# Performance work log

Measured on AMD Instinct MI355X. Metric: run time of the kernel, lower is better.

## Reference

```python
import jax, jax.numpy as jnp
import numpy as np

IN_FEATURES = 4096
OUT_FEATURES = 4096
NUM_CLUSTERS = 65536
CLUSTER_DIM = 4
DEFICIENCY = (CLUSTER_DIM - OUT_FEATURES % CLUSTER_DIM) % CLUSTER_DIM  # 0 here
INDEX_LEN = IN_FEATURES * (OUT_FEATURES + DEFICIENCY) // CLUSTER_DIM


def setup_inputs() -> dict:
    key = jax.random.key(0)
    k_x, k_c, k_i, k_b = jax.random.split(key, 4)
    x = jax.random.normal(k_x, (4, 2048, IN_FEATURES), dtype=jnp.float32)
    cluster = jax.random.normal(k_c, (NUM_CLUSTERS, CLUSTER_DIM), dtype=jnp.float32)
    index = jax.random.randint(k_i, (INDEX_LEN,), 0, NUM_CLUSTERS, dtype=jnp.int32)
    bias = jax.random.normal(k_b, (OUT_FEATURES,), dtype=jnp.float32)
    return {"x": x, "cluster": cluster, "index": index, "bias": bias}


def reference(x, cluster, index, bias):
    # Gather codebook vectors and reassemble the weight matrix [in, out(+pad)]
    vectors = cluster[index]                              # [INDEX_LEN, CLUSTER_DIM]
    weight = vectors.reshape(IN_FEATURES, -1)             # [in, out + deficiency]
    if DEFICIENCY > 0:
        weight = weight[:, :-DEFICIENCY]                  # crop padding columns
    # x: [B, S, in] @ weight: [in, out] -> [B, S, out]
    out = jnp.matmul(x, weight) + bias
    return out
```

## Files before the change

kernel.cpp:

```cpp
#include <hip/hip_runtime.h>
#include <hip/hip_bf16.h>
#include <stdint.h>

typedef unsigned short u16;
typedef __attribute__((ext_vector_type(8))) short bf16x8;
typedef __attribute__((ext_vector_type(4))) float f32x4;

#define KD 4096
#define ND 4096
#define MD 8192
#define NKT 64

__device__ __forceinline__ u16 f2bf(float f) {
    uint32_t u = __float_as_uint(f);
    u += 0x7FFFu + ((u >> 16) & 1u);
    return (u16)(u >> 16);
}

__device__ __forceinline__ void gload_lds16(const u16* g, u16* l) {
    __builtin_amdgcn_global_load_lds(
        (const __attribute__((address_space(1))) void*)g,
        (__attribute__((address_space(3))) void*)l, 16, 0, 0);
}

__global__ __launch_bounds__(256) void prep(
    const int* __restrict__ index, const float4* __restrict__ cluster4,
    u16* __restrict__ wt,
    const float4* __restrict__ x4, uint4* __restrict__ xb) {
    __shared__ int idx_s[64][32];
    const int bid = blockIdx.x;
    const int t   = threadIdx.x;
    if (bid < 2048) {
        const int k0 = (bid & 63) * 64;
        const int g0 = (bid >> 6) * 32;
        #pragma unroll
        for (int r = 0; r < 8; ++r) {
            int k = (t >> 5) + r * 8;
            int g = t & 31;
            idx_s[k][g] = index[(size_t)(k0 + k) * 1024 + g0 + g];
        }
        __syncthreads();
        const int g_local = t >> 3;
        const int k_local = (t & 7) * 8;
        u16 pk[4][8];
        #pragma unroll
        for (int j = 0; j < 8; ++j) {
            int idx = idx_s[k_local + j][g_local];
            float4 v = cluster4[idx];
            pk[0][j] = f2bf(v.x);
            pk[1][j] = f2bf(v.y);
            pk[2][j] = f2bf(v.z);
            pk[3][j] = f2bf(v.w);
        }
        const size_t nbase = (size_t)g0 * 4 + g_local * 4;
        #pragma unroll
        for (int c = 0; c < 4; ++c) {
            *reinterpret_cast<uint4*>(wt + (nbase + c) * KD + k0 + k_local) =
                *reinterpret_cast<const uint4*>(pk[c]);
        }
    } else {
        int i = (bid - 2048) * 256 + t;
        float4 a = x4[2 * i];
        float4 b = x4[2 * i + 1];
        u16 r[8] = {f2bf(a.x), f2bf(a.y), f2bf(a.z), f2bf(a.w),
                    f2bf(b.x), f2bf(b.y), f2bf(b.z), f2bf(b.w)};
        xb[i] = *reinterpret_cast<const uint4*>(r);
    }
}

__global__ __launch_bounds__(512, 2) void gemm256(
    const u16* __restrict__ A,
    const u16* __restrict__ Bt,
    const float* __restrict__ bias,
    float* __restrict__ C) {
    __shared__ __align__(16) u16 lds[65536];

    const int t    = threadIdx.x;
    const int lane = t & 63;
    const int wave = t >> 6;
    const int wm   = wave >> 2;
    const int wn   = wave & 3;

    const int bid = blockIdx.x;
    const int swz = (bid & 7) * 64 + (bid >> 3);
    const int n0  = (swz & 15) * 256;
    const int m0  = (swz >> 4) * 256;

    const u16* srcA[2]; const u16* srcB[2];
    #pragma unroll
    for (int i = 0; i < 2; ++i) {
        int p   = i * 8192 + t * 16;
        int row = p >> 7;
        int cb  = (p & 127) ^ ((row & 7) << 4);
        srcA[i] = A  + (size_t)(m0 + row) * KD + (cb >> 1);
        srcB[i] = Bt + (size_t)(n0 + row) * KD + (cb >> 1);
    }
    const size_t HS = (size_t)128 * KD;

    const int frow = lane & 15;
    int ce2[2];
    #pragma unroll
    for (int s = 0; s < 2; ++s)
        ce2[s] = ((s * 64 + ((lane >> 4) * 16)) ^ ((lane & 7) << 4)) >> 1;

    f32x4 acc[8][4] = {};
    bf16x8 aS[2][4][2];
    bf16x8 bR[2][2];

#define STAGE(isB, b, h, kt) do {                                          \
    _Pragma("unroll")                                                      \
    for (int i_ = 0; i_ < 2; ++i_) {                                       \
        const u16* s_ = ((isB) ? srcB[i_] : srcA[i_])                      \
                        + (size_t)(h) * HS + (kt) * 64;                    \
        u16* d_ = (u16*)lds + (b) * 32768 + (isB) * 16384                  \
                  + (h) * 8192 + i_ * 4096 + t * 8;                        \
        gload_lds16(s_, d_);                                               \
    } } while (0)

#define READA(b, mh) do {                                                  \
    _Pragma("unroll") for (int f_ = 0; f_ < 4; ++f_)                       \
    _Pragma("unroll") for (int s_ = 0; s_ < 2; ++s_)                       \
        aS[mh][f_][s_] = *(const bf16x8*)((u16*)lds + (b) * 32768 +        \
            ((wm * 128 + (mh) * 64 + f_ * 16 + frow) * 64) + ce2[s_]);     \
    } while (0)

#define READB(b, nh) do {                                                  \
    _Pragma("unroll") for (int g_ = 0; g_ < 2; ++g_)                       \
    _Pragma("unroll") for (int s_ = 0; s_ < 2; ++s_)                       \
        bR[g_][s_] = *(const bf16x8*)((u16*)lds + (b) * 32768 + 16384 +    \
            ((wn * 64 + (nh) * 32 + g_ * 16 + frow) * 64) + ce2[s_]);      \
    } while (0)

#define MFMA16(mh, nh) do {                                                \
    _Pragma("unroll") for (int f_ = 0; f_ < 4; ++f_)                       \
    _Pragma("unroll") for (int g_ = 0; g_ < 2; ++g_)                       \
    _Pragma("unroll") for (int s_ = 0; s_ < 2; ++s_)                       \
        acc[(mh)*4+f_][(nh)*2+g_] = __builtin_amdgcn_mfma_f32_16x16x32_bf16( \
            aS[mh][f_][s_], bR[g_][s_], acc[(mh)*4+f_][(nh)*2+g_], 0,0,0); \
    } while (0)

#define BAR() __builtin_amdgcn_s_barrier()
#define WAIT_LGKM() do { asm volatile("s_waitcnt lgkmcnt(0)" ::: "memory"); \
                         __builtin_amdgcn_sched_barrier(0); } while (0)
#define HINT_LGKM8() asm volatile("s_waitcnt lgkmcnt(8)" ::: "memory")
#define WAIT_VM4() asm volatile("s_waitcnt vmcnt(4)" ::: "memory")
#define PRIO1() __builtin_amdgcn_s_setprio(1)
#define PRIO0() __builtin_amdgcn_s_setprio(0)

    STAGE(0, 0, 0, 0);
    STAGE(0, 0, 1, 0);
    STAGE(1, 0, 0, 0);
    STAGE(1, 0, 1, 0);
    STAGE(1, 1, 0, 1);
    STAGE(0, 1, 0, 1);
    WAIT_VM4();
    BAR();

    for (int I = 0; I < NKT / 2; ++I) {
        const int tb  = 2 * I + 1;
        const int tp2 = (2 * I + 2) & (NKT - 1);
        const int tp3 = (2 * I + 3) & (NKT - 1);

        READA(0, 0); READB(0, 0); STAGE(0, 1, 1, tb);
        HINT_LGKM8();
        BAR(); WAIT_LGKM();
        PRIO1(); MFMA16(0, 0); PRIO0();
        READA(0, 1);
        BAR();
        STAGE(1, 1, 1, tb);
        BAR(); WAIT_LGKM();
        PRIO1(); MFMA16(1, 0); PRIO0();
        READB(0, 1);
        BAR();
        STAGE(1, 0, 0, tp2);
        BAR(); WAIT_LGKM();
        PRIO1(); MFMA16(0, 1); PRIO0();
        BAR();
        STAGE(0, 0, 0, tp2);
        BAR(); WAIT_LGKM();
        PRIO1(); MFMA16(1, 1); PRIO0();
        WAIT_VM4();
        BAR();
        READA(1, 0); READB(1, 0); STAGE(0, 0, 1, tp2);
        HINT_LGKM8();
        BAR(); WAIT_LGKM();
        PRIO1(); MFMA16(0, 0); PRIO0();
        READA(1, 1);
        BAR();
        STAGE(1, 0, 1, tp2);
        BAR(); WAIT_LGKM();
        PRIO1(); MFMA16(1, 0); PRIO0();
        READB(1, 1);
        BAR();
        STAGE(1, 1, 0, tp3);
        BAR(); WAIT_LGKM();
        PRIO1(); MFMA16(0, 1); PRIO0();
        BAR();
        STAGE(0, 1, 0, tp3);
        BAR(); WAIT_LGKM();
        PRIO1(); MFMA16(1, 1); PRIO0();
        WAIT_VM4();
        BAR();
    }

    const int crow = (lane >> 4) * 4;
    float bv[4];
    #pragma unroll
    for (int g = 0; g < 4; ++g)
        bv[g] = bias[n0 + wn * 64 + g * 16 + frow];
    #pragma unroll
    for (int f = 0; f < 8; ++f) {
        const int mrow = m0 + wm * 128 + f * 16 + crow;
        #pragma unroll
        for (int g = 0; g < 4; ++g) {
            float* cp = C + (size_t)mrow * ND + n0 + wn * 64 + g * 16 + frow;
            #pragma unroll
            for (int r = 0; r < 4; ++r)
                cp[(size_t)r * ND] = acc[f][g][r] + bv[g];
        }
    }
#undef STAGE
#undef READA
#undef READB
#undef MFMA16
#undef BAR
#undef WAIT_LGKM
#undef HINT_LGKM8
#undef WAIT_VM4
}

__global__ __launch_bounds__(256) void fallback_gemm(
    const float* __restrict__ x, const float4* __restrict__ cluster4,
    const int* __restrict__ index, const float* __restrict__ bias,
    float* __restrict__ out) {
    const int m = blockIdx.y;
    const int g = blockIdx.x * 256 + threadIdx.x;
    const float* xr = x + (size_t)m * KD;
    float a0 = 0.f, a1 = 0.f, a2 = 0.f, a3 = 0.f;
    for (int k = 0; k < KD; ++k) {
        float xv = xr[k];
        float4 cv = cluster4[index[(size_t)k * 1024 + g]];
        a0 += xv * cv.x; a1 += xv * cv.y; a2 += xv * cv.z; a3 += xv * cv.w;
    }
    size_t o = (size_t)m * ND + (size_t)g * 4;
    out[o + 0] = a0 + bias[g * 4 + 0];
    out[o + 1] = a1 + bias[g * 4 + 1];
    out[o + 2] = a2 + bias[g * 4 + 2];
    out[o + 3] = a3 + bias[g * 4 + 3];
}

extern "C" void kernel_launch(void* const* d_in, const int* in_sizes, int n_in,
                              void* d_out, int out_size, void* d_ws, size_t ws_size,
                              hipStream_t stream) {
    const float* x       = (const float*)d_in[0];
    const float* cluster = (const float*)d_in[1];
    const int*   index   = (const int*)d_in[2];
    const float* bias    = (const float*)d_in[3];
    float* out = (float*)d_out;

    const size_t WT_BYTES = (size_t)ND * KD * sizeof(u16);
    const size_t XB_BYTES = (size_t)MD * KD * sizeof(u16);

    if (ws_size >= WT_BYTES + XB_BYTES) {
        u16* wt = (u16*)d_ws;
        u16* xb = (u16*)((char*)d_ws + WT_BYTES);
        prep<<<2048 + (MD * KD / 8) / 256, 256, 0, stream>>>(
            index, (const float4*)cluster, wt, (const float4*)x, (uint4*)xb);
        gemm256<<<dim3((MD / 256) * (ND / 256)), 512, 0, stream>>>(
            xb, wt, bias, out);
    } else {
        fallback_gemm<<<dim3(1024 / 256, MD), 256, 0, stream>>>(
            x, (const float4*)cluster, index, bias, out);
    }
}
```

Before: 272.1 us.

## Fuse fp32-to-bf16 activation conversion into GEMM A-tile loading

Removes the separate pass that converted x to bf16 in workspace. The GEMM now loads fp32 x rows into registers, converts them to bf16 and writes swizzled tiles to LDS, interleaved with the existing B global_load_lds pipeline. This saves the extra write and read of the bf16 copy of x, but doubles A-side global read bytes per tile, adds VGPR pressure and conversion ALU inside the main loop, and complicates the vmcnt accounting.

```diff
diff --git a/kernel.cpp b/kernel.cpp
--- a/kernel.cpp
+++ b/kernel.cpp
@@ -23,53 +23,42 @@
         (__attribute__((address_space(3))) void*)l, 16, 0, 0);
 }
 
-__global__ __launch_bounds__(256) void prep(
+__global__ __launch_bounds__(256) void build_wt(
     const int* __restrict__ index, const float4* __restrict__ cluster4,
-    u16* __restrict__ wt,
-    const float4* __restrict__ x4, uint4* __restrict__ xb) {
+    u16* __restrict__ wt) {
     __shared__ int idx_s[64][32];
-    const int bid = blockIdx.x;
-    const int t   = threadIdx.x;
-    if (bid < 2048) {
-        const int k0 = (bid & 63) * 64;
-        const int g0 = (bid >> 6) * 32;
-        #pragma unroll
-        for (int r = 0; r < 8; ++r) {
-            int k = (t >> 5) + r * 8;
-            int g = t & 31;
-            idx_s[k][g] = index[(size_t)(k0 + k) * 1024 + g0 + g];
-        }
-        __syncthreads();
-        const int g_local = t >> 3;
-        const int k_local = (t & 7) * 8;
-        u16 pk[4][8];
-        #pragma unroll
-        for (int j = 0; j < 8; ++j) {
-            int idx = idx_s[k_local + j][g_local];
-            float4 v = cluster4[idx];
-            pk[0][j] = f2bf(v.x);
-            pk[1][j] = f2bf(v.y);
-            pk[2][j] = f2bf(v.z);
-            pk[3][j] = f2bf(v.w);
-        }
-        const size_t nbase = (size_t)g0 * 4 + g_local * 4;
-        #pragma unroll
-        for (int c = 0; c < 4; ++c) {
-            *reinterpret_cast<uint4*>(wt + (nbase + c) * KD + k0 + k_local) =
-                *reinterpret_cast<const uint4*>(pk[c]);
-        }
-    } else {
-        int i = (bid - 2048) * 256 + t;
-        float4 a = x4[2 * i];
-        float4 b = x4[2 * i + 1];
-        u16 r[8] = {f2bf(a.x), f2bf(a.y), f2bf(a.z), f2bf(a.w),
-                    f2bf(b.x), f2bf(b.y), f2bf(b.z), f2bf(b.w)};
-        xb[i] = *reinterpret_cast<const uint4*>(r);
+    const int t  = threadIdx.x;
+    const int k0 = blockIdx.x * 64;
+    const int g0 = blockIdx.y * 32;
+    #pragma unroll
+    for (int r = 0; r < 8; ++r) {
+        int k = (t >> 5) + r * 8;
+        int g = t & 31;
+        idx_s[k][g] = index[(size_t)(k0 + k) * 1024 + g0 + g];
+    }
+    __syncthreads();
+    const int g_local = t >> 3;
+    const int k_local = (t & 7) * 8;
+    u16 pk[4][8];
+    #pragma unroll
+    for (int j = 0; j < 8; ++j) {
+        int idx = idx_s[k_local + j][g_local];
+        float4 v = cluster4[idx];
+        pk[0][j] = f2bf(v.x);
+        pk[1][j] = f2bf(v.y);
+        pk[2][j] = f2bf(v.z);
+        pk[3][j] = f2bf(v.w);
+    }
+    const size_t nbase = (size_t)g0 * 4 + g_local * 4;
+    #pragma unroll
+    for (int c = 0; c < 4; ++c) {
+        *reinterpret_cast<uint4*>(wt + (nbase + c) * KD + k0 + k_local) =
+            *reinterpret_cast<const uint4*>(pk[c]);
     }
 }
 
 __global__ __launch_bounds__(512, 2) void gemm256(
-    const u16* __restrict__ A,
+    const float* __restrict__ X,
     const u16* __restrict__ Bt,
     const float* __restrict__ bias,
     float* __restrict__ C) {
@@ -86,16 +75,19 @@
     const int n0  = (swz & 15) * 256;
     const int m0  = (swz >> 4) * 256;
 
-    const u16* srcA[2]; const u16* srcB[2];
+    const u16* srcB[2];
     #pragma unroll
     for (int i = 0; i < 2; ++i) {
         int p   = i * 8192 + t * 16;
         int row = p >> 7;
         int cb  = (p & 127) ^ ((row & 7) << 4);
-        srcA[i] = A  + (size_t)(m0 + row) * KD + (cb >> 1);
         srcB[i] = Bt + (size_t)(n0 + row) * KD + (cb >> 1);
     }
     const size_t HS = (size_t)128 * KD;
+
+    const int arow = t >> 3;
+    const int acol = (t & 7) * 8;
+    const int aswz = acol ^ ((arow & 7) * 8);
 
     const int frow = lane & 15;
     int ce2[2];
@@ -106,15 +98,35 @@
     f32x4 acc[8][4] = {};
     bf16x8 aS[2][4][2];
     bf16x8 bR[2][2];
-
-#define STAGE(isB, b, h, kt) do {                                          \
+    float4 rX[4], rY[4];
+
+#define ALOAD(R, h, kt) do {                                               \
     _Pragma("unroll")                                                      \
     for (int i_ = 0; i_ < 2; ++i_) {                                       \
-        const u16* s_ = ((isB) ? srcB[i_] : srcA[i_])                      \
-                        + (size_t)(h) * HS + (kt) * 64;                    \
-        u16* d_ = (u16*)lds + (b) * 32768 + (isB) * 16384                  \
-                  + (h) * 8192 + i_ * 4096 + t * 8;                        \
-        gload_lds16(s_, d_);                                               \
+        const float* s_ = X + (size_t)(m0 + (h) * 128 + i_ * 64 + arow)    \
+                          * KD + (kt) * 64 + acol;                         \
+        R[2 * i_]     = *(const float4*)(s_);                              \
+        R[2 * i_ + 1] = *(const float4*)(s_ + 4);                          \
+    } } while (0)
+
+#define AWRITE(R, b, h) do {                                               \
+    _Pragma("unroll")                                                      \
+    for (int i_ = 0; i_ < 2; ++i_) {                                       \
+        u16 pk_[8];                                                        \
+        const float* f_ = (const float*)&R[2 * i_];                        \
+        _Pragma("unroll")                                                  \
+        for (int j_ = 0; j_ < 8; ++j_) pk_[j_] = f2bf(f_[j_]);             \
+        *(bf16x8*)((u16*)lds + (b) * 32768 + (h) * 8192 +                  \
+                   (i_ * 64 + arow) * 64 + aswz) =                         \
+            *(const bf16x8*)pk_;                                           \
+    } } while (0)
+
+#define STAGEB(b, h, kt) do {                                              \
+    _Pragma("unroll")                                                      \
+    for (int i_ = 0; i_ < 2; ++i_) {                                       \
+        gload_lds16(srcB[i_] + (size_t)(h) * HS + (kt) * 64,               \
+                    (u16*)lds + (b) * 32768 + 16384 + (h) * 8192 +         \
+                    i_ * 4096 + t * 8);                                    \
     } } while (0)
 
 #define READA(b, mh) do {                                                  \
@@ -142,18 +154,23 @@
 #define BAR() __builtin_amdgcn_s_barrier()
 #define WAIT_LGKM() do { asm volatile("s_waitcnt lgkmcnt(0)" ::: "memory"); \
                          __builtin_amdgcn_sched_barrier(0); } while (0)
-#define HINT_LGKM8() asm volatile("s_waitcnt lgkmcnt(8)" ::: "memory")
-#define WAIT_VM4() asm volatile("s_waitcnt vmcnt(4)" ::: "memory")
+#define WVM(N) asm volatile("s_waitcnt vmcnt(" #N ")" ::: "memory")
 #define PRIO1() __builtin_amdgcn_s_setprio(1)
 #define PRIO0() __builtin_amdgcn_s_setprio(0)
 
-    STAGE(0, 0, 0, 0);
-    STAGE(0, 0, 1, 0);
-    STAGE(1, 0, 0, 0);
-    STAGE(1, 0, 1, 0);
-    STAGE(1, 1, 0, 1);
-    STAGE(0, 1, 0, 1);
-    WAIT_VM4();
+    ALOAD(rX, 0, 0);
+    ALOAD(rY, 1, 0);
+    STAGEB(0, 0, 0);
+    STAGEB(0, 1, 0);
+    WVM(4);
+    AWRITE(rX, 0, 0);
+    AWRITE(rY, 0, 1);
+    ALOAD(rX, 0, 1);
+    ALOAD(rY, 1, 1);
+    STAGEB(1, 0, 1);
+    WVM(6);
+    AWRITE(rX, 1, 0);
+    WAIT_LGKM();
     BAR();
 
     for (int I = 0; I < NKT / 2; ++I) {
@@ -161,45 +178,51 @@
         const int tp2 = (2 * I + 2) & (NKT - 1);
         const int tp3 = (2 * I + 3) & (NKT - 1);
 
-        READA(0, 0); READB(0, 0); STAGE(0, 1, 1, tb);
-        HINT_LGKM8();
+        READA(0, 0); READB(0, 0);
         BAR(); WAIT_LGKM();
         PRIO1(); MFMA16(0, 0); PRIO0();
+        WVM(2);
+        AWRITE(rY, 1, 1);
         READA(0, 1);
         BAR();
-        STAGE(1, 1, 1, tb);
+        STAGEB(1, 1, tb);
+        ALOAD(rX, 0, tp2);
         BAR(); WAIT_LGKM();
         PRIO1(); MFMA16(1, 0); PRIO0();
         READB(0, 1);
         BAR();
-        STAGE(1, 0, 0, tp2);
+        ALOAD(rY, 1, tp2);
+        STAGEB(0, 0, tp2);
         BAR(); WAIT_LGKM();
         PRIO1(); MFMA16(0, 1); PRIO0();
         BAR();
-        STAGE(0, 0, 0, tp2);
         BAR(); WAIT_LGKM();
         PRIO1(); MFMA16(1, 1); PRIO0();
-        WAIT_VM4();
-        BAR();
-        READA(1, 0); READB(1, 0); STAGE(0, 0, 1, tp2);
-        HINT_LGKM8();
+        WVM(6);
+        AWRITE(rX, 0, 0);
+        BAR();
+        READA(1, 0); READB(1, 0);
         BAR(); WAIT_LGKM();
         PRIO1(); MFMA16(0, 0); PRIO0();
+        WVM(2);
+        AWRITE(rY, 0, 1);
+        ALOAD(rX, 0, tp3);
         READA(1, 1);
         BAR();
-        STAGE(1, 0, 1, tp2);
+        STAGEB(0, 1, tp2);
         BAR(); WAIT_LGKM();
         PRIO1(); MFMA16(1, 0); PRIO0();
         READB(1, 1);
         BAR();
-        STAGE(1, 1, 0, tp3);
+        ALOAD(rY, 1, tp3);
+        STAGEB(1, 0, tp3);
         BAR(); WAIT_LGKM();
         PRIO1(); MFMA16(0, 1); PRIO0();
         BAR();
-        STAGE(0, 1, 0, tp3);
         BAR(); WAIT_LGKM();
         PRIO1(); MFMA16(1, 1); PRIO0();
-        WAIT_VM4();
+        WVM(6);
+        AWRITE(rX, 1, 0);
         BAR();
     }
 
@@ -219,14 +242,15 @@
                 cp[(size_t)r * ND] = acc[f][g][r] + bv[g];
         }
     }
-#undef STAGE
+#undef ALOAD
+#undef AWRITE
+#undef STAGEB
 #undef READA
 #undef READB
 #undef MFMA16
 #undef BAR
 #undef WAIT_LGKM
-#undef HINT_LGKM8
-#undef WAIT_VM4
+#undef WVM
 }
 
 __global__ __launch_bounds__(256) void fallback_gemm(
@@ -259,15 +283,13 @@
     float* out = (float*)d_out;
 
     const size_t WT_BYTES = (size_t)ND * KD * sizeof(u16);
-    const size_t XB_BYTES = (size_t)MD * KD * sizeof(u16);
-
-    if (ws_size >= WT_BYTES + XB_BYTES) {
+
+    if (ws_size >= WT_BYTES) {
         u16* wt = (u16*)d_ws;
-        u16* xb = (u16*)((char*)d_ws + WT_BYTES);
-        prep<<<2048 + (MD * KD / 8) / 256, 256, 0, stream>>>(
-            index, (const float4*)cluster, wt, (const float4*)x, (uint4*)xb);
+        build_wt<<<dim3(KD / 64, ND / 128), 256, 0, stream>>>(
+            index, (const float4*)cluster, wt);
         gemm256<<<dim3((MD / 256) * (ND / 256)), 512, 0, stream>>>(
-            xb, wt, bias, out);
+            x, wt, bias, out);
     } else {
         fallback_gemm<<<dim3(1024 / 256, MD), 256, 0, stream>>>(
             x, (const float4*)cluster, index, bias, out);
```

New measurement: 769.8 us. +182.9%, slower.
